# Kernel tuning notes

Hardware: AMD Instinct MI355X
Metric: run time of the kernel (lower is better)

Reference implementation:

```python
import jax, jax.numpy as jnp
import numpy as np

N, E, R, D = 50000, 800000, 8, 64
BN_EPS = 1e-5


def _bn_relu(x, g, b):
    # training-mode BatchNorm1d (biased variance) + relu
    m = x.mean(axis=0)
    v = x.var(axis=0)
    return jax.nn.relu((x - m) / jnp.sqrt(v + BN_EPS) * g + b)


def setup_inputs() -> dict:
    key = jax.random.key(0)
    ks = jax.random.split(key, 10)
    return {
        'x': jax.random.normal(ks[0], (N, D), dtype=jnp.float32),
        'edge_weight': jax.random.uniform(ks[1], (E,), dtype=jnp.float32),
        'W_lin1': jax.random.normal(ks[2], (D, R * D), dtype=jnp.float32) * 0.05,
        'b_lin1': jnp.zeros((D,), jnp.float32),
        'W_self1': jax.random.normal(ks[3], (D, D), dtype=jnp.float32) * 0.05,
        'b_self1': jnp.zeros((D,), jnp.float32),
        'gamma1': jnp.ones((D,), jnp.float32),
        'beta1': jnp.zeros((D,), jnp.float32),
        'W_lin2': jax.random.normal(ks[4], (D, D), dtype=jnp.float32) * 0.05,
        'b_lin2': jnp.zeros((D,), jnp.float32),
        'W_self2': jax.random.normal(ks[5], (D, D), dtype=jnp.float32) * 0.05,
        'b_self2': jnp.zeros((D,), jnp.float32),
        'gamma2': jnp.ones((D,), jnp.float32),
        'beta2': jnp.zeros((D,), jnp.float32),
        'node_in': jax.random.randint(ks[6], (E,), 0, N, dtype=jnp.int32),
        'node_out': jax.random.randint(ks[7], (E,), 0, N, dtype=jnp.int32),
        'relation': jax.random.randint(ks[8], (E,), 0, R, dtype=jnp.int32),
        'num_relation': R,
    }


def reference(x, edge_weight, W_lin1, b_lin1, W_self1, b_self1, gamma1, beta1,
              W_lin2, b_lin2, W_self2, b_self2, gamma2, beta2,
              node_in, node_out, relation, num_relation):
    Nn, Din = x.shape
    Rr = int(num_relation)
    seg = node_out * Rr + relation  # node_out * num_relation + relation
    # degree normalization of edge weights (shared by both layers)
    deg = jax.ops.segment_sum(edge_weight, seg, num_segments=Nn * Rr)
    ew = edge_weight / deg[seg]

    # layer 1: relationalGraphConv
    msgs = x[node_in] * ew[:, None]  # [E, D]
    upd = jax.ops.segment_sum(msgs, seg, num_segments=Nn * Rr)
    upd = upd.reshape(Nn, Rr * Din)  # node-major flatten, matches torch .view
    h = upd @ W_lin1.T + b_lin1 + x @ W_self1.T + b_self1
    h = _bn_relu(h, gamma1, beta1)  # [N, D]

    # layer 2: relationalGraph (per-relation outputs)
    msgs2 = h[node_in] * ew[:, None]
    upd2 = jax.ops.segment_sum(msgs2, seg, num_segments=Nn * Rr)  # [N*R, D] node-major
    upd2 = upd2.reshape(Nn, Rr, -1).transpose(1, 0, 2).reshape(Rr * Nn, -1)  # relation-major
    h_rep = jnp.tile(h, (Rr, 1))  # input.repeat(R, 1)
    out = upd2 @ W_lin2.T + b_lin2 + h_rep @ W_self2.T + b_self2
    out = _bn_relu(out, gamma2, beta2)
    return out.reshape(Rr, Nn, -1)
```

## Files before the change

kernel.cpp:

```cpp
#include <hip/hip_runtime.h>


#define GATHER_GRID 2048
#define SCAN_CHUNK 4096
#define RED_BLOCKS 64
#define PREP_BLOCKS 16
#define COUNT_BLOCKS 2048
#define PLACE_BLOCKS 1024

typedef short bf16x8 __attribute__((ext_vector_type(8)));
typedef float f32x4 __attribute__((ext_vector_type(4)));

static __device__ __forceinline__ float bf2f(unsigned short u) {
  return __uint_as_float(((unsigned)u) << 16);
}
static __device__ __forceinline__ unsigned short f2bf(float f) {
  unsigned u = __float_as_uint(f);
  u += 0x7FFFu + ((u >> 16) & 1u);
  return (unsigned short)(u >> 16);
}

__global__ void k_zero(int* __restrict__ cnt, int n) {
  int i = blockIdx.x * blockDim.x + threadIdx.x;
  int stride = gridDim.x * blockDim.x;
  for (int k = i; k < n; k += stride) cnt[k] = 0;
}

__global__ void k_countprep(const int* __restrict__ node_out, const int* __restrict__ rel,
                            int* __restrict__ cnt, int* __restrict__ tmp, int E, int R,
                            const float* __restrict__ Wlin1, const float* __restrict__ Wself1,
                            const float* __restrict__ Wlin2, const float* __restrict__ Wself2,
                            unsigned short* __restrict__ wb1, unsigned short* __restrict__ wb2) {
  if (blockIdx.x < PREP_BLOCKS) {
    int i = blockIdx.x * 256 + threadIdx.x;
    int stride = PREP_BLOCKS * 256;
    int n1 = (R + 1) * 64 * 64;
    int n2 = 2 * 64 * 64;
    for (int k = i; k < n1 + n2; k += stride) {
      if (k < n1) {
        int r = k >> 6, d = k & 63;
        float v;
        if (r < R * 64) {
          int s = r >> 6, j = r & 63;
          v = Wlin1[j * (R * 64) + s * 64 + d];
        } else {
          v = Wself1[(r - R * 64) * 64 + d];
        }
        wb1[k] = f2bf(v);
      } else {
        int k2 = k - n1;
        int r = k2 >> 6, d = k2 & 63;
        float v = (r < 64) ? Wlin2[r * 64 + d] : Wself2[(r - 64) * 64 + d];
        wb2[k2] = f2bf(v);
      }
    }
  } else {
    int i = (blockIdx.x - PREP_BLOCKS) * 256 + threadIdx.x;
    int stride = COUNT_BLOCKS * 256;
    for (int e = i; e < E; e += stride) {
      int seg = node_out[e] * R + rel[e];
      tmp[e] = atomicAdd(&cnt[seg], 1);
    }
  }
}

__global__ __launch_bounds__(256) void k_scan1(const int* __restrict__ cnt,
                                               int* __restrict__ bsum, int NR) {
  __shared__ int red[256];
  int tid = threadIdx.x;
  int base = blockIdx.x * SCAN_CHUNK;
  int s = 0;
  for (int i = tid; i < SCAN_CHUNK; i += 256) {
    int idx = base + i;
    if (idx < NR) s += cnt[idx];
  }
  red[tid] = s;
  __syncthreads();
  for (int off = 128; off > 0; off >>= 1) {
    if (tid < off) red[tid] += red[tid + off];
    __syncthreads();
  }
  if (tid == 0) bsum[blockIdx.x] = red[0];
}

__global__ void k_scan2(const int* __restrict__ bsum, int* __restrict__ bpre,
                        int* __restrict__ rowptr_end, int NB) {
  int lane = threadIdx.x;
  int carry = 0;
  for (int base = 0; base < NB; base += 64) {
    int i = base + lane;
    int v = (i < NB) ? bsum[i] : 0;
    int incl = v;
    #pragma unroll
    for (int off = 1; off < 64; off <<= 1) {
      int u = __shfl_up(incl, off);
      if (lane >= off) incl += u;
    }
    if (i < NB) bpre[i] = carry + incl - v;
    carry += __shfl(incl, 63);
  }
  if (lane == 0) *rowptr_end = carry;
}

__global__ __launch_bounds__(256) void k_scan3(const int* __restrict__ cnt,
                                               const int* __restrict__ bpre,
                                               int* __restrict__ rowptr, int NR) {
  __shared__ int wtot[4];
  int tid = threadIdx.x, lane = tid & 63, wid = tid >> 6;
  int base = blockIdx.x * SCAN_CHUNK + tid * 16;
  int v[16];
  int t = 0;
  #pragma unroll
  for (int i = 0; i < 16; i++) {
    int idx = base + i;
    v[i] = (idx < NR) ? cnt[idx] : 0;
    t += v[i];
  }
  int incl = t;
  #pragma unroll
  for (int off = 1; off < 64; off <<= 1) {
    int u = __shfl_up(incl, off);
    if (lane >= off) incl += u;
  }
  if (lane == 63) wtot[wid] = incl;
  __syncthreads();
  int woff = 0;
  for (int w = 0; w < wid; w++) woff += wtot[w];
  int start = bpre[blockIdx.x] + woff + incl - t;
  #pragma unroll
  for (int i = 0; i < 16; i++) {
    int idx = base + i;
    if (idx < NR) rowptr[idx] = start;
    start += v[i];
  }
}

__global__ __launch_bounds__(256) void k_placegemm(
    const float* __restrict__ w, const int* __restrict__ node_out,
    const int* __restrict__ node_in, const int* __restrict__ rel,
    const int* __restrict__ rowptr, const int* __restrict__ tmp,
    int2* __restrict__ ep, int E, int R,
    const float* __restrict__ xf, int M, const unsigned short* __restrict__ Wb,
    int nslab, unsigned short* __restrict__ outLinB, unsigned short* __restrict__ outSelf,
    int mblocks) {
  if ((int)blockIdx.x < mblocks) {
    int m0 = blockIdx.x * 64;
    int wid = threadIdx.x >> 6;
    int lane = threadIdx.x & 63;
    int mrow = m0 + wid * 16 + (lane & 15);
    int mload = (mrow < M) ? mrow : (M - 1);
    const float* arow = xf + (size_t)mload * 64 + 8 * (lane >> 4);
    float4 af0 = *(const float4*)(arow);
    float4 af1 = *(const float4*)(arow + 4);
    float4 af2 = *(const float4*)(arow + 32);
    float4 af3 = *(const float4*)(arow + 36);
    bf16x8 a0, a1;
    a0[0] = (short)f2bf(af0.x); a0[1] = (short)f2bf(af0.y);
    a0[2] = (short)f2bf(af0.z); a0[3] = (short)f2bf(af0.w);
    a0[4] = (short)f2bf(af1.x); a0[5] = (short)f2bf(af1.y);
    a0[6] = (short)f2bf(af1.z); a0[7] = (short)f2bf(af1.w);
    a1[0] = (short)f2bf(af2.x); a1[1] = (short)f2bf(af2.y);
    a1[2] = (short)f2bf(af2.z); a1[3] = (short)f2bf(af2.w);
    a1[4] = (short)f2bf(af3.x); a1[5] = (short)f2bf(af3.y);
    a1[6] = (short)f2bf(af3.z); a1[7] = (short)f2bf(af3.w);
    int rbase = m0 + wid * 16 + ((lane >> 4) << 2);
    int cbase = lane & 15;
    for (int slab = 0; slab <= nslab; ++slab) {
      const unsigned short* wrow = Wb + ((size_t)slab * 64 + (lane & 15)) * 64 + 8 * (lane >> 4);
      unsigned short* op = (slab < nslab) ? (outLinB + (size_t)slab * M * 64) : outSelf;
      #pragma unroll
      for (int nt = 0; nt < 4; ++nt) {
        bf16x8 b0 = *(const bf16x8*)(wrow + nt * 16 * 64);
        bf16x8 b1 = *(const bf16x8*)(wrow + nt * 16 * 64 + 32);
        f32x4 c = {};
        c = __builtin_amdgcn_mfma_f32_16x16x32_bf16(a0, b0, c, 0, 0, 0);
        c = __builtin_amdgcn_mfma_f32_16x16x32_bf16(a1, b1, c, 0, 0, 0);
        int col = nt * 16 + cbase;
        #pragma unroll
        for (int rg = 0; rg < 4; ++rg) {
          int grow = rbase + rg;
          if (grow < M) op[(size_t)grow * 64 + col] = f2bf(c[rg]);
        }
      }
    }
  } else {
    int i = ((int)blockIdx.x - mblocks) * 256 + threadIdx.x;
    int stride = PLACE_BLOCKS * 256;
    for (int e = i; e < E; e += stride) {
      int rr = rel[e];
      int seg = node_out[e] * R + rr;
      int pos = rowptr[seg] + tmp[e];
      ep[pos] = make_int2(node_in[e] | (rr << 16), __float_as_int(w[e]));
    }
  }
}

__global__ void k_norm(const int* __restrict__ rowptr, int2* __restrict__ ep, int NR) {
  int s = blockIdx.x * blockDim.x + threadIdx.x;
  if (s >= NR) return;
  int k0 = rowptr[s], k1 = rowptr[s + 1];
  if (k0 >= k1) return;
  float d = 0.f;
  for (int k = k0; k < k1; k++) d += __int_as_float(ep[k].y);
  float inv = 1.f / d;
  for (int k = k0; k < k1; k++) {
    int2 v = ep[k];
    v.y = __float_as_int(__int_as_float(v.y) * inv);
    ep[k] = v;
  }
}

__global__ __launch_bounds__(256) void k_gemm2bn(
    const unsigned short* __restrict__ hp, int M,
    const unsigned short* __restrict__ Wb, int nslab,
    const float* __restrict__ ss,
    unsigned short* __restrict__ outLinB, unsigned short* __restrict__ outSelf) {
  __shared__ float sss[128];
  if (threadIdx.x < 128) sss[threadIdx.x] = ss[threadIdx.x];
  __syncthreads();
  int m0 = blockIdx.x * 64;
  int wid = threadIdx.x >> 6;
  int lane = threadIdx.x & 63;
  int mrow = m0 + wid * 16 + (lane & 15);
  int mload = (mrow < M) ? mrow : (M - 1);
  int cb = 8 * (lane >> 4);
  const unsigned short* arow = hp + (size_t)mload * 64 + cb;
  ushort4 u0 = *(const ushort4*)(arow);
  ushort4 u1 = *(const ushort4*)(arow + 4);
  ushort4 u2 = *(const ushort4*)(arow + 32);
  ushort4 u3 = *(const ushort4*)(arow + 36);
  bf16x8 a0, a1;
  #pragma unroll
  for (int j = 0; j < 4; j++) {
    unsigned short uu0 = (&u0.x)[j], uu1 = (&u1.x)[j], uu2 = (&u2.x)[j], uu3 = (&u3.x)[j];
    a0[j]     = (short)f2bf(fmaxf(fmaf(bf2f(uu0), sss[cb + j],      sss[64 + cb + j]), 0.f));
    a0[j + 4] = (short)f2bf(fmaxf(fmaf(bf2f(uu1), sss[cb + 4 + j],  sss[64 + cb + 4 + j]), 0.f));
    a1[j]     = (short)f2bf(fmaxf(fmaf(bf2f(uu2), sss[cb + 32 + j], sss[64 + cb + 32 + j]), 0.f));
    a1[j + 4] = (short)f2bf(fmaxf(fmaf(bf2f(uu3), sss[cb + 36 + j], sss[64 + cb + 36 + j]), 0.f));
  }
  int rbase = m0 + wid * 16 + ((lane >> 4) << 2);
  int cbase = lane & 15;
  for (int slab = 0; slab <= nslab; ++slab) {
    const unsigned short* wrow = Wb + ((size_t)slab * 64 + (lane & 15)) * 64 + 8 * (lane >> 4);
    unsigned short* op = (slab < nslab) ? (outLinB + (size_t)slab * M * 64) : outSelf;
    #pragma unroll
    for (int nt = 0; nt < 4; ++nt) {
      bf16x8 b0 = *(const bf16x8*)(wrow + nt * 16 * 64);
      bf16x8 b1 = *(const bf16x8*)(wrow + nt * 16 * 64 + 32);
      f32x4 c = {};
      c = __builtin_amdgcn_mfma_f32_16x16x32_bf16(a0, b0, c, 0, 0, 0);
      c = __builtin_amdgcn_mfma_f32_16x16x32_bf16(a1, b1, c, 0, 0, 0);
      int col = nt * 16 + cbase;
      #pragma unroll
      for (int rg = 0; rg < 4; ++rg) {
        int grow = rbase + rg;
        if (grow < M) op[(size_t)grow * 64 + col] = f2bf(c[rg]);
      }
    }
  }
}

__global__ __launch_bounds__(256) void k_gather1(
    const int* __restrict__ rowptr, const int2* __restrict__ ep,
    const unsigned short* __restrict__ y1, const unsigned short* __restrict__ s1,
    unsigned short* __restrict__ h_pre, float* __restrict__ part, int N, int R) {
  int lane = threadIdx.x & 63;
  int wid = threadIdx.x >> 6;
  int l16 = lane & 15;
  int lg = lane >> 4;
  int c0 = l16 * 4;
  int grp = blockIdx.x * 16 + wid * 4 + lg;
  int ngrp = gridDim.x * 16;
  float lsum[4] = {0.f, 0.f, 0.f, 0.f}, lsq[4] = {0.f, 0.f, 0.f, 0.f};
  for (int n = grp; n < N; n += ngrp) {
    int k = rowptr[n * R];
    int k1 = rowptr[n * R + R];
    float a0 = 0.f, a1 = 0.f, a2 = 0.f, a3 = 0.f;
    for (; k + 1 < k1; k += 2) {
      int2 pA = ep[k];
      int2 pB = ep[k + 1];
      ushort4 uA = *(const ushort4*)&y1[((size_t)((pA.x >> 16) * N + (pA.x & 0xFFFF))) * 64 + c0];
      ushort4 uB = *(const ushort4*)&y1[((size_t)((pB.x >> 16) * N + (pB.x & 0xFFFF))) * 64 + c0];
      float wA = __int_as_float(pA.y), wB = __int_as_float(pB.y);
      a0 = fmaf(wA, bf2f(uA.x), a0); a1 = fmaf(wA, bf2f(uA.y), a1);
      a2 = fmaf(wA, bf2f(uA.z), a2); a3 = fmaf(wA, bf2f(uA.w), a3);
      a0 = fmaf(wB, bf2f(uB.x), a0); a1 = fmaf(wB, bf2f(uB.y), a1);
      a2 = fmaf(wB, bf2f(uB.z), a2); a3 = fmaf(wB, bf2f(uB.w), a3);
    }
    if (k < k1) {
      int2 p = ep[k];
      float w = __int_as_float(p.y);
      ushort4 u = *(const ushort4*)&y1[((size_t)((p.x >> 16) * N + (p.x & 0xFFFF))) * 64 + c0];
      a0 = fmaf(w, bf2f(u.x), a0); a1 = fmaf(w, bf2f(u.y), a1);
      a2 = fmaf(w, bf2f(u.z), a2); a3 = fmaf(w, bf2f(u.w), a3);
    }
    ushort4 su = *(const ushort4*)&s1[(size_t)n * 64 + c0];
    float v0 = a0 + bf2f(su.x), v1 = a1 + bf2f(su.y);
    float v2 = a2 + bf2f(su.z), v3 = a3 + bf2f(su.w);
    ushort4 o; o.x = f2bf(v0); o.y = f2bf(v1); o.z = f2bf(v2); o.w = f2bf(v3);
    *(ushort4*)&h_pre[(size_t)n * 64 + c0] = o;
    lsum[0] += v0; lsq[0] += v0 * v0;
    lsum[1] += v1; lsq[1] += v1 * v1;
    lsum[2] += v2; lsq[2] += v2 * v2;
    lsum[3] += v3; lsq[3] += v3 * v3;
  }
  __shared__ float sp[16][64], sq[16][64];
  int g = wid * 4 + lg;
  #pragma unroll
  for (int i = 0; i < 4; i++) { sp[g][c0 + i] = lsum[i]; sq[g][c0 + i] = lsq[i]; }
  __syncthreads();
  if (threadIdx.x < 64) {
    int j = threadIdx.x;
    float s = 0.f, q = 0.f;
    #pragma unroll
    for (int gg = 0; gg < 16; gg++) { s += sp[gg][j]; q += sq[gg][j]; }
    part[(size_t)blockIdx.x * 128 + j] = s;
    part[(size_t)blockIdx.x * 128 + 64 + j] = q;
  }
}

__global__ __launch_bounds__(256) void k_gather2_stats(
    const int* __restrict__ rowptr, const int2* __restrict__ ep,
    const unsigned short* __restrict__ z, const unsigned short* __restrict__ s2,
    float* __restrict__ part, int N, int R) {
  int lane = threadIdx.x & 63;
  int wid = threadIdx.x >> 6;
  int l16 = lane & 15;
  int lg = lane >> 4;
  int c0 = l16 * 4;
  int grp = blockIdx.x * 16 + wid * 4 + lg;
  int ngrp = gridDim.x * 16;
  int NR = N * R;
  float lsum[4] = {0.f, 0.f, 0.f, 0.f}, lsq[4] = {0.f, 0.f, 0.f, 0.f};
  for (int s = grp; s < NR; s += ngrp) {
    unsigned r = (unsigned)s / (unsigned)N;
    int n = s - (int)r * N;
    int seg = n * R + (int)r;
    int k = rowptr[seg];
    int k1 = rowptr[seg + 1];
    float a0 = 0.f, a1 = 0.f, a2 = 0.f, a3 = 0.f;
    for (; k + 1 < k1; k += 2) {
      int2 pA = ep[k];
      int2 pB = ep[k + 1];
      ushort4 uA = *(const ushort4*)&z[(size_t)(pA.x & 0xFFFF) * 64 + c0];
      ushort4 uB = *(const ushort4*)&z[(size_t)(pB.x & 0xFFFF) * 64 + c0];
      float wA = __int_as_float(pA.y), wB = __int_as_float(pB.y);
      a0 = fmaf(wA, bf2f(uA.x), a0); a1 = fmaf(wA, bf2f(uA.y), a1);
      a2 = fmaf(wA, bf2f(uA.z), a2); a3 = fmaf(wA, bf2f(uA.w), a3);
      a0 = fmaf(wB, bf2f(uB.x), a0); a1 = fmaf(wB, bf2f(uB.y), a1);
      a2 = fmaf(wB, bf2f(uB.z), a2); a3 = fmaf(wB, bf2f(uB.w), a3);
    }
    if (k < k1) {
      int2 p = ep[k];
      float w = __int_as_float(p.y);
      ushort4 u = *(const ushort4*)&z[(size_t)(p.x & 0xFFFF) * 64 + c0];
      a0 = fmaf(w, bf2f(u.x), a0); a1 = fmaf(w, bf2f(u.y), a1);
      a2 = fmaf(w, bf2f(u.z), a2); a3 = fmaf(w, bf2f(u.w), a3);
    }
    ushort4 su = *(const ushort4*)&s2[(size_t)n * 64 + c0];
    float v0 = a0 + bf2f(su.x), v1 = a1 + bf2f(su.y);
    float v2 = a2 + bf2f(su.z), v3 = a3 + bf2f(su.w);
    lsum[0] += v0; lsq[0] += v0 * v0;
    lsum[1] += v1; lsq[1] += v1 * v1;
    lsum[2] += v2; lsq[2] += v2 * v2;
    lsum[3] += v3; lsq[3] += v3 * v3;
  }
  __shared__ float sp[16][64], sq[16][64];
  int g = wid * 4 + lg;
  #pragma unroll
  for (int i = 0; i < 4; i++) { sp[g][c0 + i] = lsum[i]; sq[g][c0 + i] = lsq[i]; }
  __syncthreads();
  if (threadIdx.x < 64) {
    int j = threadIdx.x;
    float s = 0.f, q = 0.f;
    #pragma unroll
    for (int gg = 0; gg < 16; gg++) { s += sp[gg][j]; q += sq[gg][j]; }
    part[(size_t)blockIdx.x * 128 + j] = s;
    part[(size_t)blockIdx.x * 128 + 64 + j] = q;
  }
}

__global__ __launch_bounds__(256) void k_gather2_write(
    const int* __restrict__ rowptr, const int2* __restrict__ ep,
    const unsigned short* __restrict__ z, const unsigned short* __restrict__ s2,
    const float* __restrict__ ss, float* __restrict__ out, int N, int R) {
  int lane = threadIdx.x & 63;
  int wid = threadIdx.x >> 6;
  int l16 = lane & 15;
  int lg = lane >> 4;
  int c0 = l16 * 4;
  float sc0 = ss[c0], sc1 = ss[c0 + 1], sc2 = ss[c0 + 2], sc3 = ss[c0 + 3];
  float sh0 = ss[64 + c0], sh1 = ss[64 + c0 + 1], sh2 = ss[64 + c0 + 2], sh3 = ss[64 + c0 + 3];
  int grp = blockIdx.x * 16 + wid * 4 + lg;
  int ngrp = gridDim.x * 16;
  int NR = N * R;
  for (int s = grp; s < NR; s += ngrp) {
    unsigned r = (unsigned)s / (unsigned)N;
    int n = s - (int)r * N;
    int seg = n * R + (int)r;
    int k = rowptr[seg];
    int k1 = rowptr[seg + 1];
    float a0 = 0.f, a1 = 0.f, a2 = 0.f, a3 = 0.f;
    for (; k + 1 < k1; k += 2) {
      int2 pA = ep[k];
      int2 pB = ep[k + 1];
      ushort4 uA = *(const ushort4*)&z[(size_t)(pA.x & 0xFFFF) * 64 + c0];
      ushort4 uB = *(const ushort4*)&z[(size_t)(pB.x & 0xFFFF) * 64 + c0];
      float wA = __int_as_float(pA.y), wB = __int_as_float(pB.y);
      a0 = fmaf(wA, bf2f(uA.x), a0); a1 = fmaf(wA, bf2f(uA.y), a1);
      a2 = fmaf(wA, bf2f(uA.z), a2); a3 = fmaf(wA, bf2f(uA.w), a3);
      a0 = fmaf(wB, bf2f(uB.x), a0); a1 = fmaf(wB, bf2f(uB.y), a1);
      a2 = fmaf(wB, bf2f(uB.z), a2); a3 = fmaf(wB, bf2f(uB.w), a3);
    }
    if (k < k1) {
      int2 p = ep[k];
      float w = __int_as_float(p.y);
      ushort4 u = *(const ushort4*)&z[(size_t)(p.x & 0xFFFF) * 64 + c0];
      a0 = fmaf(w, bf2f(u.x), a0); a1 = fmaf(w, bf2f(u.y), a1);
      a2 = fmaf(w, bf2f(u.z), a2); a3 = fmaf(w, bf2f(u.w), a3);
    }
    ushort4 su = *(const ushort4*)&s2[(size_t)n * 64 + c0];
    float v0 = fmaxf(fmaf(a0 + bf2f(su.x), sc0, sh0), 0.f);
    float v1 = fmaxf(fmaf(a1 + bf2f(su.y), sc1, sh1), 0.f);
    float v2 = fmaxf(fmaf(a2 + bf2f(su.z), sc2, sh2), 0.f);
    float v3 = fmaxf(fmaf(a3 + bf2f(su.w), sc3, sh3), 0.f);
    *(float4*)&out[(size_t)s * 64 + c0] = make_float4(v0, v1, v2, v3);
  }
}

__global__ __launch_bounds__(256) void k_red1(const float* __restrict__ part,
                                              float* __restrict__ part2, int P) {
  int j = threadIdx.x & 127;
  int g = threadIdx.x >> 7;
  int rows = P / RED_BLOCKS;
  int base = blockIdx.x * rows;
  float acc = 0.f;
  for (int i = g; i < rows; i += 2) acc += part[(size_t)(base + i) * 128 + j];
  __shared__ float red[2][128];
  red[g][j] = acc;
  __syncthreads();
  if (threadIdx.x < 128) part2[(size_t)blockIdx.x * 128 + j] = red[0][j] + red[1][j];
}

__global__ __launch_bounds__(1024) void k_bnstats(
    const float* __restrict__ part, int P, float M,
    const float* __restrict__ gamma, const float* __restrict__ beta,
    float* __restrict__ ss) {
  __shared__ float red[1024];
  int tid = threadIdx.x;
  int j = tid & 127;
  int g = tid >> 7;
  float acc = 0.f;
  for (int i = g; i < P; i += 8) acc += part[(size_t)i * 128 + j];
  red[tid] = acc;
  __syncthreads();
  if (tid < 128) {
    float s = 0.f;
    for (int gg = 0; gg < 8; gg++) s += red[gg * 128 + tid];
    red[tid] = s;
  }
  __syncthreads();
  if (tid < 64) {
    float s = red[tid], q = red[64 + tid];
    float mean = s / M;
    float var = q / M - mean * mean;
    float sc = gamma[tid] / sqrtf(var + 1e-5f);
    ss[tid] = sc;
    ss[64 + tid] = beta[tid] - mean * sc;
  }
}

extern "C" void kernel_launch(void* const* d_in, const int* in_sizes, int n_in,
                              void* d_out, int out_size, void* d_ws, size_t ws_size,
                              hipStream_t stream) {
  const float* x        = (const float*)d_in[0];
  const float* edge_w   = (const float*)d_in[1];
  const float* W_lin1   = (const float*)d_in[2];
  const float* W_self1  = (const float*)d_in[4];
  const float* gamma1   = (const float*)d_in[6];
  const float* beta1    = (const float*)d_in[7];
  const float* W_lin2   = (const float*)d_in[8];
  const float* W_self2  = (const float*)d_in[10];
  const float* gamma2   = (const float*)d_in[12];
  const float* beta2    = (const float*)d_in[13];
  const int* node_in    = (const int*)d_in[14];
  const int* node_out   = (const int*)d_in[15];
  const int* relation   = (const int*)d_in[16];

  int N = in_sizes[0] / 64;
  int E = in_sizes[1];
  int R = in_sizes[2] / (64 * 64);
  int NR = N * R;
  int NB = (NR + SCAN_CHUNK - 1) / SCAN_CHUNK;

  char* p = (char*)d_ws;
  auto alloc = [&](size_t bytes) { char* r = p; p += (bytes + 255) & ~(size_t)255; return r; };
  int* cnt      = (int*)alloc(4ull * NR);
  int* rowptr   = (int*)alloc(4ull * (NR + 1));
  int* tmp      = (int*)alloc(4ull * E);
  int* bsum     = (int*)alloc(4ull * NB);
  int* bpre     = (int*)alloc(4ull * NB);
  int2* ep      = (int2*)alloc(8ull * E);
  unsigned short* wb1 = (unsigned short*)alloc(2ull * (R + 1) * 64 * 64);
  unsigned short* wb2 = (unsigned short*)alloc(2ull * 2 * 64 * 64);
  unsigned short* s1    = (unsigned short*)alloc(2ull * N * 64);
  unsigned short* h_pre = (unsigned short*)alloc(2ull * N * 64);
  unsigned short* z     = (unsigned short*)alloc(2ull * N * 64);
  unsigned short* s2    = (unsigned short*)alloc(2ull * N * 64);
  float* part   = (float*)alloc(4ull * GATHER_GRID * 128);
  float* part2  = (float*)alloc(4ull * RED_BLOCKS * 128);
  float* ss1    = (float*)alloc(4ull * 128);
  float* ss2    = (float*)alloc(4ull * 128);

  unsigned short* y1 = (unsigned short*)d_out;

  int mblocks = (N + 63) / 64;

  k_zero<<<256, 256, 0, stream>>>(cnt, NR);
  k_countprep<<<PREP_BLOCKS + COUNT_BLOCKS, 256, 0, stream>>>(
      node_out, relation, cnt, tmp, E, R, W_lin1, W_self1, W_lin2, W_self2, wb1, wb2);
  k_scan1<<<NB, 256, 0, stream>>>(cnt, bsum, NR);
  k_scan2<<<1, 64, 0, stream>>>(bsum, bpre, &rowptr[NR], NB);
  k_scan3<<<NB, 256, 0, stream>>>(cnt, bpre, rowptr, NR);
  k_placegemm<<<mblocks + PLACE_BLOCKS, 256, 0, stream>>>(
      edge_w, node_out, node_in, relation, rowptr, tmp, ep, E, R,
      x, N, wb1, R, y1, s1, mblocks);
  k_norm<<<(NR + 255) / 256, 256, 0, stream>>>(rowptr, ep, NR);

  k_gather1<<<GATHER_GRID, 256, 0, stream>>>(rowptr, ep, y1, s1, h_pre, part, N, R);
  k_red1<<<RED_BLOCKS, 256, 0, stream>>>(part, part2, GATHER_GRID);
  k_bnstats<<<1, 1024, 0, stream>>>(part2, RED_BLOCKS, (float)N, gamma1, beta1, ss1);

  k_gemm2bn<<<mblocks, 256, 0, stream>>>(h_pre, N, wb2, 1, ss1, z, s2);
  k_gather2_stats<<<GATHER_GRID, 256, 0, stream>>>(rowptr, ep, z, s2, part, N, R);
  k_red1<<<RED_BLOCKS, 256, 0, stream>>>(part, part2, GATHER_GRID);
  k_bnstats<<<1, 1024, 0, stream>>>(part2, RED_BLOCKS, (float)N * R, gamma2, beta2, ss2);
  k_gather2_write<<<GATHER_GRID, 256, 0, stream>>>(rowptr, ep, z, s2, ss2, (float*)d_out, N, R);
}
```

Measured before the change: 257.7 us.

## Fold degree normalization into gathers and regroup prep kernels around the GEMM

Removes the separate k_norm pass and instead computes each segment's weight sum and its reciprocal inside the gather kernels, which then scale edge weights on the fly. The layer-1 MFMA GEMM now runs in the same launch as the edge-count atomics rather than with placement, and zeroing is merged with weight packing. The relation bits are no longer packed into node_in, and gather1 iterates relations explicitly. Each segment's edge weights are now summed again in every gather pass (three times), and segment sums are computed per thread redundantly across the 16 lanes sharing a node.

```diff
diff --git a/kernel.cpp b/kernel.cpp
--- a/kernel.cpp
+++ b/kernel.cpp
@@ -4,7 +4,8 @@
 #define GATHER_GRID 2048
 #define SCAN_CHUNK 4096
 #define RED_BLOCKS 64
-#define PREP_BLOCKS 16
+#define ZERO_BLOCKS 256
+#define PACK_BLOCKS 16
 #define COUNT_BLOCKS 2048
 #define PLACE_BLOCKS 1024
 
@@ -20,20 +21,17 @@
   return (unsigned short)(u >> 16);
 }
 
-__global__ void k_zero(int* __restrict__ cnt, int n) {
-  int i = blockIdx.x * blockDim.x + threadIdx.x;
-  int stride = gridDim.x * blockDim.x;
-  for (int k = i; k < n; k += stride) cnt[k] = 0;
-}
-
-__global__ void k_countprep(const int* __restrict__ node_out, const int* __restrict__ rel,
-                            int* __restrict__ cnt, int* __restrict__ tmp, int E, int R,
-                            const float* __restrict__ Wlin1, const float* __restrict__ Wself1,
-                            const float* __restrict__ Wlin2, const float* __restrict__ Wself2,
-                            unsigned short* __restrict__ wb1, unsigned short* __restrict__ wb2) {
-  if (blockIdx.x < PREP_BLOCKS) {
+__global__ void k_zeropack(int* __restrict__ cnt, int NR, int R,
+                           const float* __restrict__ Wlin1, const float* __restrict__ Wself1,
+                           const float* __restrict__ Wlin2, const float* __restrict__ Wself2,
+                           unsigned short* __restrict__ wb1, unsigned short* __restrict__ wb2) {
+  if (blockIdx.x < ZERO_BLOCKS) {
     int i = blockIdx.x * 256 + threadIdx.x;
-    int stride = PREP_BLOCKS * 256;
+    int stride = ZERO_BLOCKS * 256;
+    for (int k = i; k < NR; k += stride) cnt[k] = 0;
+  } else {
+    int i = (blockIdx.x - ZERO_BLOCKS) * 256 + threadIdx.x;
+    int stride = PACK_BLOCKS * 256;
     int n1 = (R + 1) * 64 * 64;
     int n2 = 2 * 64 * 64;
     for (int k = i; k < n1 + n2; k += stride) {
@@ -54,94 +52,14 @@
         wb2[k2] = f2bf(v);
       }
     }
-  } else {
-    int i = (blockIdx.x - PREP_BLOCKS) * 256 + threadIdx.x;
-    int stride = COUNT_BLOCKS * 256;
-    for (int e = i; e < E; e += stride) {
-      int seg = node_out[e] * R + rel[e];
-      tmp[e] = atomicAdd(&cnt[seg], 1);
-    }
-  }
-}
-
-__global__ __launch_bounds__(256) void k_scan1(const int* __restrict__ cnt,
-                                               int* __restrict__ bsum, int NR) {
-  __shared__ int red[256];
-  int tid = threadIdx.x;
-  int base = blockIdx.x * SCAN_CHUNK;
-  int s = 0;
-  for (int i = tid; i < SCAN_CHUNK; i += 256) {
-    int idx = base + i;
-    if (idx < NR) s += cnt[idx];
-  }
-  red[tid] = s;
-  __syncthreads();
-  for (int off = 128; off > 0; off >>= 1) {
-    if (tid < off) red[tid] += red[tid + off];
-    __syncthreads();
-  }
-  if (tid == 0) bsum[blockIdx.x] = red[0];
-}
-
-__global__ void k_scan2(const int* __restrict__ bsum, int* __restrict__ bpre,
-                        int* __restrict__ rowptr_end, int NB) {
-  int lane = threadIdx.x;
-  int carry = 0;
-  for (int base = 0; base < NB; base += 64) {
-    int i = base + lane;
-    int v = (i < NB) ? bsum[i] : 0;
-    int incl = v;
-    #pragma unroll
-    for (int off = 1; off < 64; off <<= 1) {
-      int u = __shfl_up(incl, off);
-      if (lane >= off) incl += u;
-    }
-    if (i < NB) bpre[i] = carry + incl - v;
-    carry += __shfl(incl, 63);
-  }
-  if (lane == 0) *rowptr_end = carry;
-}
-
-__global__ __launch_bounds__(256) void k_scan3(const int* __restrict__ cnt,
-                                               const int* __restrict__ bpre,
-                                               int* __restrict__ rowptr, int NR) {
-  __shared__ int wtot[4];
-  int tid = threadIdx.x, lane = tid & 63, wid = tid >> 6;
-  int base = blockIdx.x * SCAN_CHUNK + tid * 16;
-  int v[16];
-  int t = 0;
-  #pragma unroll
-  for (int i = 0; i < 16; i++) {
-    int idx = base + i;
-    v[i] = (idx < NR) ? cnt[idx] : 0;
-    t += v[i];
-  }
-  int incl = t;
-  #pragma unroll
-  for (int off = 1; off < 64; off <<= 1) {
-    int u = __shfl_up(incl, off);
-    if (lane >= off) incl += u;
-  }
-  if (lane == 63) wtot[wid] = incl;
-  __syncthreads();
-  int woff = 0;
-  for (int w = 0; w < wid; w++) woff += wtot[w];
-  int start = bpre[blockIdx.x] + woff + incl - t;
-  #pragma unroll
-  for (int i = 0; i < 16; i++) {
-    int idx = base + i;
-    if (idx < NR) rowptr[idx] = start;
-    start += v[i];
-  }
-}
-
-__global__ __launch_bounds__(256) void k_placegemm(
-    const float* __restrict__ w, const int* __restrict__ node_out,
-    const int* __restrict__ node_in, const int* __restrict__ rel,
-    const int* __restrict__ rowptr, const int* __restrict__ tmp,
-    int2* __restrict__ ep, int E, int R,
+  }
+}
+
+__global__ __launch_bounds__(256) void k_countgemm(
+    const int* __restrict__ node_out, const int* __restrict__ rel,
+    int* __restrict__ cnt, int* __restrict__ tmp, int E, int R,
     const float* __restrict__ xf, int M, const unsigned short* __restrict__ Wb,
-    int nslab, unsigned short* __restrict__ outLinB, unsigned short* __restrict__ outSelf,
+    unsigned short* __restrict__ outLinB, unsigned short* __restrict__ outSelf,
     int mblocks) {
   if ((int)blockIdx.x < mblocks) {
     int m0 = blockIdx.x * 64;
@@ -165,9 +83,9 @@
     a1[6] = (short)f2bf(af3.z); a1[7] = (short)f2bf(af3.w);
     int rbase = m0 + wid * 16 + ((lane >> 4) << 2);
     int cbase = lane & 15;
-    for (int slab = 0; slab <= nslab; ++slab) {
+    for (int slab = 0; slab <= R; ++slab) {
       const unsigned short* wrow = Wb + ((size_t)slab * 64 + (lane & 15)) * 64 + 8 * (lane >> 4);
-      unsigned short* op = (slab < nslab) ? (outLinB + (size_t)slab * M * 64) : outSelf;
+      unsigned short* op = (slab < R) ? (outLinB + (size_t)slab * M * 64) : outSelf;
       #pragma unroll
       for (int nt = 0; nt < 4; ++nt) {
         bf16x8 b0 = *(const bf16x8*)(wrow + nt * 16 * 64);
@@ -185,28 +103,95 @@
     }
   } else {
     int i = ((int)blockIdx.x - mblocks) * 256 + threadIdx.x;
-    int stride = PLACE_BLOCKS * 256;
+    int stride = COUNT_BLOCKS * 256;
     for (int e = i; e < E; e += stride) {
-      int rr = rel[e];
-      int seg = node_out[e] * R + rr;
-      int pos = rowptr[seg] + tmp[e];
-      ep[pos] = make_int2(node_in[e] | (rr << 16), __float_as_int(w[e]));
-    }
-  }
-}
-
-__global__ void k_norm(const int* __restrict__ rowptr, int2* __restrict__ ep, int NR) {
-  int s = blockIdx.x * blockDim.x + threadIdx.x;
-  if (s >= NR) return;
-  int k0 = rowptr[s], k1 = rowptr[s + 1];
-  if (k0 >= k1) return;
-  float d = 0.f;
-  for (int k = k0; k < k1; k++) d += __int_as_float(ep[k].y);
-  float inv = 1.f / d;
-  for (int k = k0; k < k1; k++) {
-    int2 v = ep[k];
-    v.y = __float_as_int(__int_as_float(v.y) * inv);
-    ep[k] = v;
+      int seg = node_out[e] * R + rel[e];
+      tmp[e] = atomicAdd(&cnt[seg], 1);
+    }
+  }
+}
+
+__global__ __launch_bounds__(256) void k_scan1(const int* __restrict__ cnt,
+                                               int* __restrict__ bsum, int NR) {
+  __shared__ int red[256];
+  int tid = threadIdx.x;
+  int base = blockIdx.x * SCAN_CHUNK;
+  int s = 0;
+  for (int i = tid; i < SCAN_CHUNK; i += 256) {
+    int idx = base + i;
+    if (idx < NR) s += cnt[idx];
+  }
+  red[tid] = s;
+  __syncthreads();
+  for (int off = 128; off > 0; off >>= 1) {
+    if (tid < off) red[tid] += red[tid + off];
+    __syncthreads();
+  }
+  if (tid == 0) bsum[blockIdx.x] = red[0];
+}
+
+__global__ void k_scan2(const int* __restrict__ bsum, int* __restrict__ bpre,
+                        int* __restrict__ rowptr_end, int NB) {
+  int lane = threadIdx.x;
+  int carry = 0;
+  for (int base = 0; base < NB; base += 64) {
+    int i = base + lane;
+    int v = (i < NB) ? bsum[i] : 0;
+    int incl = v;
+    #pragma unroll
+    for (int off = 1; off < 64; off <<= 1) {
+      int u = __shfl_up(incl, off);
+      if (lane >= off) incl += u;
+    }
+    if (i < NB) bpre[i] = carry + incl - v;
+    carry += __shfl(incl, 63);
+  }
+  if (lane == 0) *rowptr_end = carry;
+}
+
+__global__ __launch_bounds__(256) void k_scan3(const int* __restrict__ cnt,
+                                               const int* __restrict__ bpre,
+                                               int* __restrict__ rowptr, int NR) {
+  __shared__ int wtot[4];
+  int tid = threadIdx.x, lane = tid & 63, wid = tid >> 6;
+  int base = blockIdx.x * SCAN_CHUNK + tid * 16;
+  int v[16];
+  int t = 0;
+  #pragma unroll
+  for (int i = 0; i < 16; i++) {
+    int idx = base + i;
+    v[i] = (idx < NR) ? cnt[idx] : 0;
+    t += v[i];
+  }
+  int incl = t;
+  #pragma unroll
+  for (int off = 1; off < 64; off <<= 1) {
+    int u = __shfl_up(incl, off);
+    if (lane >= off) incl += u;
+  }
+  if (lane == 63) wtot[wid] = incl;
+  __syncthreads();
+  int woff = 0;
+  for (int w = 0; w < wid; w++) woff += wtot[w];
+  int start = bpre[blockIdx.x] + woff + incl - t;
+  #pragma unroll
+  for (int i = 0; i < 16; i++) {
+    int idx = base + i;
+    if (idx < NR) rowptr[idx] = start;
+    start += v[i];
+  }
+}
+
+__global__ void k_place(const float* __restrict__ w, const int* __restrict__ node_out,
+                        const int* __restrict__ node_in, const int* __restrict__ rel,
+                        const int* __restrict__ rowptr, const int* __restrict__ tmp,
+                        int2* __restrict__ ep, int E, int R) {
+  int i = blockIdx.x * blockDim.x + threadIdx.x;
+  int stride = gridDim.x * blockDim.x;
+  for (int e = i; e < E; e += stride) {
+    int seg = node_out[e] * R + rel[e];
+    int pos = rowptr[seg] + tmp[e];
+    ep[pos] = make_int2(node_in[e], __float_as_int(w[e]));
   }
 }
 
@@ -273,26 +258,36 @@
   int ngrp = gridDim.x * 16;
   float lsum[4] = {0.f, 0.f, 0.f, 0.f}, lsq[4] = {0.f, 0.f, 0.f, 0.f};
   for (int n = grp; n < N; n += ngrp) {
-    int k = rowptr[n * R];
-    int k1 = rowptr[n * R + R];
+    int segbase = n * R;
+    int k = rowptr[segbase];
     float a0 = 0.f, a1 = 0.f, a2 = 0.f, a3 = 0.f;
-    for (; k + 1 < k1; k += 2) {
-      int2 pA = ep[k];
-      int2 pB = ep[k + 1];
-      ushort4 uA = *(const ushort4*)&y1[((size_t)((pA.x >> 16) * N + (pA.x & 0xFFFF))) * 64 + c0];
-      ushort4 uB = *(const ushort4*)&y1[((size_t)((pB.x >> 16) * N + (pB.x & 0xFFFF))) * 64 + c0];
-      float wA = __int_as_float(pA.y), wB = __int_as_float(pB.y);
-      a0 = fmaf(wA, bf2f(uA.x), a0); a1 = fmaf(wA, bf2f(uA.y), a1);
-      a2 = fmaf(wA, bf2f(uA.z), a2); a3 = fmaf(wA, bf2f(uA.w), a3);
-      a0 = fmaf(wB, bf2f(uB.x), a0); a1 = fmaf(wB, bf2f(uB.y), a1);
-      a2 = fmaf(wB, bf2f(uB.z), a2); a3 = fmaf(wB, bf2f(uB.w), a3);
-    }
-    if (k < k1) {
-      int2 p = ep[k];
-      float w = __int_as_float(p.y);
-      ushort4 u = *(const ushort4*)&y1[((size_t)((p.x >> 16) * N + (p.x & 0xFFFF))) * 64 + c0];
-      a0 = fmaf(w, bf2f(u.x), a0); a1 = fmaf(w, bf2f(u.y), a1);
-      a2 = fmaf(w, bf2f(u.z), a2); a3 = fmaf(w, bf2f(u.w), a3);
+    for (int r = 0; r < R; r++) {
+      int k1 = rowptr[segbase + r + 1];
+      if (k < k1) {
+        float d = 0.f;
+        for (int kk = k; kk < k1; kk++) d += __int_as_float(ep[kk].y);
+        float inv = 1.f / d;
+        const unsigned short* yb = y1 + (size_t)r * N * 64;
+        for (; k + 1 < k1; k += 2) {
+          int2 pA = ep[k];
+          int2 pB = ep[k + 1];
+          ushort4 uA = *(const ushort4*)&yb[(size_t)pA.x * 64 + c0];
+          ushort4 uB = *(const ushort4*)&yb[(size_t)pB.x * 64 + c0];
+          float wA = __int_as_float(pA.y) * inv, wB = __int_as_float(pB.y) * inv;
+          a0 = fmaf(wA, bf2f(uA.x), a0); a1 = fmaf(wA, bf2f(uA.y), a1);
+          a2 = fmaf(wA, bf2f(uA.z), a2); a3 = fmaf(wA, bf2f(uA.w), a3);
+          a0 = fmaf(wB, bf2f(uB.x), a0); a1 = fmaf(wB, bf2f(uB.y), a1);
+          a2 = fmaf(wB, bf2f(uB.z), a2); a3 = fmaf(wB, bf2f(uB.w), a3);
+        }
+        if (k < k1) {
+          int2 p = ep[k];
+          float w = __int_as_float(p.y) * inv;
+          ushort4 u = *(const ushort4*)&yb[(size_t)p.x * 64 + c0];
+          a0 = fmaf(w, bf2f(u.x), a0); a1 = fmaf(w, bf2f(u.y), a1);
+          a2 = fmaf(w, bf2f(u.z), a2); a3 = fmaf(w, bf2f(u.w), a3);
+        }
+        k = k1;
+      }
     }
     ushort4 su = *(const ushort4*)&s1[(size_t)n * 64 + c0];
     float v0 = a0 + bf2f(su.x), v1 = a1 + bf2f(su.y);
@@ -339,23 +334,28 @@
     int k = rowptr[seg];
     int k1 = rowptr[seg + 1];
     float a0 = 0.f, a1 = 0.f, a2 = 0.f, a3 = 0.f;
-    for (; k + 1 < k1; k += 2) {
-      int2 pA = ep[k];
-      int2 pB = ep[k + 1];
-      ushort4 uA = *(const ushort4*)&z[(size_t)(pA.x & 0xFFFF) * 64 + c0];
-      ushort4 uB = *(const ushort4*)&z[(size_t)(pB.x & 0xFFFF) * 64 + c0];
-      float wA = __int_as_float(pA.y), wB = __int_as_float(pB.y);
-      a0 = fmaf(wA, bf2f(uA.x), a0); a1 = fmaf(wA, bf2f(uA.y), a1);
-      a2 = fmaf(wA, bf2f(uA.z), a2); a3 = fmaf(wA, bf2f(uA.w), a3);
-      a0 = fmaf(wB, bf2f(uB.x), a0); a1 = fmaf(wB, bf2f(uB.y), a1);
-      a2 = fmaf(wB, bf2f(uB.z), a2); a3 = fmaf(wB, bf2f(uB.w), a3);
-    }
     if (k < k1) {
-      int2 p = ep[k];
-      float w = __int_as_float(p.y);
-      ushort4 u = *(const ushort4*)&z[(size_t)(p.x & 0xFFFF) * 64 + c0];
-      a0 = fmaf(w, bf2f(u.x), a0); a1 = fmaf(w, bf2f(u.y), a1);
-      a2 = fmaf(w, bf2f(u.z), a2); a3 = fmaf(w, bf2f(u.w), a3);
+      float d = 0.f;
+      for (int kk = k; kk < k1; kk++) d += __int_as_float(ep[kk].y);
+      float inv = 1.f / d;
+      for (; k + 1 < k1; k += 2) {
+        int2 pA = ep[k];
+        int2 pB = ep[k + 1];
+        ushort4 uA = *(const ushort4*)&z[(size_t)pA.x * 64 + c0];
+        ushort4 uB = *(const ushort4*)&z[(size_t)pB.x * 64 + c0];
+        float wA = __int_as_float(pA.y) * inv, wB = __int_as_float(pB.y) * inv;
+        a0 = fmaf(wA, bf2f(uA.x), a0); a1 = fmaf(wA, bf2f(uA.y), a1);
+        a2 = fmaf(wA, bf2f(uA.z), a2); a3 = fmaf(wA, bf2f(uA.w), a3);
+        a0 = fmaf(wB, bf2f(uB.x), a0); a1 = fmaf(wB, bf2f(uB.y), a1);
+        a2 = fmaf(wB, bf2f(uB.z), a2); a3 = fmaf(wB, bf2f(uB.w), a3);
+      }
+      if (k < k1) {
+        int2 p = ep[k];
+        float w = __int_as_float(p.y) * inv;
+        ushort4 u = *(const ushort4*)&z[(size_t)p.x * 64 + c0];
+        a0 = fmaf(w, bf2f(u.x), a0); a1 = fmaf(w, bf2f(u.y), a1);
+        a2 = fmaf(w, bf2f(u.z), a2); a3 = fmaf(w, bf2f(u.w), a3);
+      }
     }
     ushort4 su = *(const ushort4*)&s2[(size_t)n * 64 + c0];
     float v0 = a0 + bf2f(su.x), v1 = a1 + bf2f(su.y);
@@ -401,23 +401,28 @@
     int k = rowptr[seg];
     int k1 = rowptr[seg + 1];
     float a0 = 0.f, a1 = 0.f, a2 = 0.f, a3 = 0.f;
-    for (; k + 1 < k1; k += 2) {
-      int2 pA = ep[k];
-      int2 pB = ep[k + 1];
-      ushort4 uA = *(const ushort4*)&z[(size_t)(pA.x & 0xFFFF) * 64 + c0];
-      ushort4 uB = *(const ushort4*)&z[(size_t)(pB.x & 0xFFFF) * 64 + c0];
-      float wA = __int_as_float(pA.y), wB = __int_as_float(pB.y);
-      a0 = fmaf(wA, bf2f(uA.x), a0); a1 = fmaf(wA, bf2f(uA.y), a1);
-      a2 = fmaf(wA, bf2f(uA.z), a2); a3 = fmaf(wA, bf2f(uA.w), a3);
-      a0 = fmaf(wB, bf2f(uB.x), a0); a1 = fmaf(wB, bf2f(uB.y), a1);
-      a2 = fmaf(wB, bf2f(uB.z), a2); a3 = fmaf(wB, bf2f(uB.w), a3);
-    }
     if (k < k1) {
-      int2 p = ep[k];
-      float w = __int_as_float(p.y);
-      ushort4 u = *(const ushort4*)&z[(size_t)(p.x & 0xFFFF) * 64 + c0];
-      a0 = fmaf(w, bf2f(u.x), a0); a1 = fmaf(w, bf2f(u.y), a1);
-      a2 = fmaf(w, bf2f(u.z), a2); a3 = fmaf(w, bf2f(u.w), a3);
+      float d = 0.f;
+      for (int kk = k; kk < k1; kk++) d += __int_as_float(ep[kk].y);
+      float inv = 1.f / d;
+      for (; k + 1 < k1; k += 2) {
+        int2 pA = ep[k];
+        int2 pB = ep[k + 1];
+        ushort4 uA = *(const ushort4*)&z[(size_t)pA.x * 64 + c0];
+        ushort4 uB = *(const ushort4*)&z[(size_t)pB.x * 64 + c0];
+        float wA = __int_as_float(pA.y) * inv, wB = __int_as_float(pB.y) * inv;
+        a0 = fmaf(wA, bf2f(uA.x), a0); a1 = fmaf(wA, bf2f(uA.y), a1);
+        a2 = fmaf(wA, bf2f(uA.z), a2); a3 = fmaf(wA, bf2f(uA.w), a3);
+        a0 = fmaf(wB, bf2f(uB.x), a0); a1 = fmaf(wB, bf2f(uB.y), a1);
+        a2 = fmaf(wB, bf2f(uB.z), a2); a3 = fmaf(wB, bf2f(uB.w), a3);
+      }
+      if (k < k1) {
+        int2 p = ep[k];
+        float w = __int_as_float(p.y) * inv;
+        ushort4 u = *(const ushort4*)&z[(size_t)p.x * 64 + c0];
+        a0 = fmaf(w, bf2f(u.x), a0); a1 = fmaf(w, bf2f(u.y), a1);
+        a2 = fmaf(w, bf2f(u.z), a2); a3 = fmaf(w, bf2f(u.w), a3);
+      }
     }
     ushort4 su = *(const ushort4*)&s2[(size_t)n * 64 + c0];
     float v0 = fmaxf(fmaf(a0 + bf2f(su.x), sc0, sh0), 0.f);
@@ -516,16 +521,15 @@
 
   int mblocks = (N + 63) / 64;
 
-  k_zero<<<256, 256, 0, stream>>>(cnt, NR);
-  k_countprep<<<PREP_BLOCKS + COUNT_BLOCKS, 256, 0, stream>>>(
-      node_out, relation, cnt, tmp, E, R, W_lin1, W_self1, W_lin2, W_self2, wb1, wb2);
+  k_zeropack<<<ZERO_BLOCKS + PACK_BLOCKS, 256, 0, stream>>>(
+      cnt, NR, R, W_lin1, W_self1, W_lin2, W_self2, wb1, wb2);
+  k_countgemm<<<mblocks + COUNT_BLOCKS, 256, 0, stream>>>(
+      node_out, relation, cnt, tmp, E, R, x, N, wb1, y1, s1, mblocks);
   k_scan1<<<NB, 256, 0, stream>>>(cnt, bsum, NR);
   k_scan2<<<1, 64, 0, stream>>>(bsum, bpre, &rowptr[NR], NB);
   k_scan3<<<NB, 256, 0, stream>>>(cnt, bpre, rowptr, NR);
-  k_placegemm<<<mblocks + PLACE_BLOCKS, 256, 0, stream>>>(
-      edge_w, node_out, node_in, relation, rowptr, tmp, ep, E, R,
-      x, N, wb1, R, y1, s1, mblocks);
-  k_norm<<<(NR + 255) / 256, 256, 0, stream>>>(rowptr, ep, NR);
+  k_place<<<PLACE_BLOCKS, 256, 0, stream>>>(
+      edge_w, node_out, node_in, relation, rowptr, tmp, ep, E, R);
 
   k_gather1<<<GATHER_GRID, 256, 0, stream>>>(rowptr, ep, y1, s1, h_pre, part, N, R);
   k_red1<<<RED_BLOCKS, 256, 0, stream>>>(part, part2, GATHER_GRID);
```

Result: slower. 301.1 us (+16.8%).
